# Optimization experiments

Measured on AMD Instinct MI355X. Metric: run time of the kernel, lower is better.

## Reference

```python
import jax, jax.numpy as jnp
import numpy as np
import math

B, S, D, H = 4, 2048, 1024, 16
HD = D // H  # head dim = 64


def setup_inputs() -> dict:
    key = jax.random.key(0)
    ks = jax.random.split(key, 8)
    queries = jax.random.normal(ks[0], (B, S, D), dtype=jnp.float32)
    keys = jax.random.normal(ks[1], (B, S, D), dtype=jnp.float32)
    values = jax.random.normal(ks[2], (B, S, D), dtype=jnp.float32)
    valid_lens = jnp.maximum(jax.random.randint(ks[3], (B,), 0, S), 1).astype(jnp.int64)
    scale = 1.0 / math.sqrt(D)
    Wq = jax.random.normal(ks[4], (H, D, HD), dtype=jnp.float32) * scale
    Wk = jax.random.normal(ks[5], (H, D, HD), dtype=jnp.float32) * scale
    Wv = jax.random.normal(ks[6], (H, D, HD), dtype=jnp.float32) * scale
    Wo = jax.random.normal(ks[7], (H * HD, D), dtype=jnp.float32) * scale
    return {"queries": queries, "keys": keys, "values": values,
            "valid_lens": valid_lens, "Wq": Wq, "Wk": Wk, "Wv": Wv, "Wo": Wo}


def reference(queries, keys, values, valid_lens, Wq, Wk, Wv, Wo):
    # Per-head projections, batched over heads: [B,S,D] x [H,D,HD] -> [B,H,S,HD]
    q = jnp.einsum('bsd,hde->bhse', queries, Wq)
    k = jnp.einsum('bsd,hde->bhse', keys, Wk)
    v = jnp.einsum('bsd,hde->bhse', values, Wv)
    # Scaled dot-product scores: [B,H,S,S]
    scores = jnp.einsum('bhse,bhte->bhst', q, k) / jnp.sqrt(jnp.float32(HD))
    # Padding mask only (causal=False default in the torch forward)
    pad = jnp.arange(S)[None, :] >= valid_lens[:, None]  # [B,S] True = masked
    scores = jnp.where(pad[:, None, None, :], -jnp.inf, scores)
    attn = jax.nn.softmax(scores, axis=-1)
    out = jnp.einsum('bhst,bhte->bhse', attn, v)  # [B,H,S,HD]
    out = out.transpose(0, 2, 1, 3).reshape(q.shape[0], S, H * HD)  # concat heads
    return out @ Wo
```

## Files before the change

### kernel.cpp

```cpp
#include <hip/hip_runtime.h>
#include <hip/hip_bf16.h>

typedef __bf16 bf16;
typedef __attribute__((ext_vector_type(8))) __bf16 bf16x8;
typedef __attribute__((ext_vector_type(4))) float f32x4;

#define DEV __device__ __forceinline__

DEV float fexp2(float x) {
#if __has_builtin(__builtin_amdgcn_exp2f)
  return __builtin_amdgcn_exp2f(x);
#else
  return exp2f(x);
#endif
}

DEV void gload_lds16(const void* g, void* l) {
  __builtin_amdgcn_global_load_lds(
      (__attribute__((address_space(1))) void*)(g),
      (__attribute__((address_space(3))) void*)(l), 16, 0, 0);
}

__global__ void k_cvt_act(const float* __restrict__ q, const float* __restrict__ k,
                          const float* __restrict__ v, bf16* __restrict__ qb,
                          bf16* __restrict__ kb, bf16* __restrict__ vb) {
  const int bid = blockIdx.x;
  const int which = bid >> 12;
  const float* in = which == 0 ? q : which == 1 ? k : v;
  bf16* out = which == 0 ? qb : which == 1 ? kb : vb;
  const int i = (bid & 4095) * 256 + threadIdx.x;
  const float4* p = reinterpret_cast<const float4*>(in) + (size_t)i * 2;
  float4 a = p[0], b = p[1];
  bf16x8 o;
  o[0] = (bf16)a.x; o[1] = (bf16)a.y; o[2] = (bf16)a.z; o[3] = (bf16)a.w;
  o[4] = (bf16)b.x; o[5] = (bf16)b.y; o[6] = (bf16)b.z; o[7] = (bf16)b.w;
  *reinterpret_cast<bf16x8*>(out + (size_t)i * 8) = o;
}

__global__ void k_cvt_w(const float* __restrict__ Wq, const float* __restrict__ Wk,
                        const float* __restrict__ Wv, const float* __restrict__ Wo,
                        bf16* __restrict__ WqkvT, bf16* __restrict__ WoT) {
  const int idx = blockIdx.x * blockDim.x + threadIdx.x;
  const int which = idx >> 20, r = idx & ((1 << 20) - 1);
  if (which < 3) {
    const float* W = which == 0 ? Wq : which == 1 ? Wk : Wv;
    const int d = r & 1023, n = r >> 10;
    float val = W[((size_t)(n >> 6) << 16) + (size_t)d * 64 + (n & 63)];
    if (which == 0) val *= 0.180336880f;
    WqkvT[((size_t)which << 20) + r] = (bf16)val;
  } else {
    const int kk = r & 1023, n = r >> 10;
    WoT[r] = (bf16)Wo[(size_t)kk * 1024 + n];
  }
}

__global__ __launch_bounds__(256) void k_gemm_qkv(const bf16* __restrict__ qA,
                                                  const bf16* __restrict__ kA,
                                                  const bf16* __restrict__ vA,
                                                  const bf16* __restrict__ Wt,
                                                  bf16* __restrict__ Qh,
                                                  bf16* __restrict__ Kh,
                                                  bf16* __restrict__ Vt) {
  constexpr int K = 1024;
  __shared__ __align__(16) bf16 As[128 * 32];
  __shared__ __align__(16) bf16 Bs[128 * 32];
  const int tid = threadIdx.x;
  const int lane = tid & 63, w = tid >> 6;
  const int wr = w >> 1, wc = w & 1;
  const int lgrp = lane >> 4, lid = lane & 15;
  const int m0 = blockIdx.x * 128;
  const int n0g = blockIdx.y * 128;
  const int proj = n0g >> 10, n0 = n0g & 1023;
  const bf16* A = proj == 0 ? qA : proj == 1 ? kA : vA;
  const bf16* Bt = Wt + (size_t)n0g * K;

  f32x4 acc[4][4] = {};

  const int c0 = w * 2, c1 = w * 2 + 1;
  const int bo0 = c0 * 1024 + lane * 16, bo1 = c1 * 1024 + lane * 16;
  const int r0 = bo0 >> 6, e0 = (bo0 & 63) >> 1;
  const int r1 = bo1 >> 6, e1 = (bo1 & 63) >> 1;

  for (int k0 = 0; k0 < K; k0 += 32) {
    __syncthreads();
    gload_lds16(A + (size_t)(m0 + r0) * K + k0 + e0, (char*)As + c0 * 1024);
    gload_lds16(A + (size_t)(m0 + r1) * K + k0 + e1, (char*)As + c1 * 1024);
    gload_lds16(Bt + (size_t)r0 * K + k0 + e0, (char*)Bs + c0 * 1024);
    gload_lds16(Bt + (size_t)r1 * K + k0 + e1, (char*)Bs + c1 * 1024);
    __syncthreads();
    bf16x8 af[4], bfv[4];
    for (int m = 0; m < 4; ++m)
      af[m] = *reinterpret_cast<const bf16x8*>(&As[(wr * 64 + m * 16 + lid) * 32 + lgrp * 8]);
    for (int n = 0; n < 4; ++n)
      bfv[n] = *reinterpret_cast<const bf16x8*>(&Bs[(wc * 64 + n * 16 + lid) * 32 + lgrp * 8]);
    for (int m = 0; m < 4; ++m)
      for (int n = 0; n < 4; ++n)
        acc[m][n] = __builtin_amdgcn_mfma_f32_16x16x32_bf16(af[m], bfv[n], acc[m][n], 0, 0, 0);
  }

  if (proj == 0) {
    for (int m = 0; m < 4; ++m) {
      int rowb = m0 + wr * 64 + m * 16 + lgrp * 4;
      for (int n = 0; n < 4; ++n) {
        int col = n0 + wc * 64 + n * 16 + lid;
        int h = col >> 6, e = col & 63;
        for (int r = 0; r < 4; ++r) {
          int row = rowb + r;
          int b = row >> 11, s = row & 2047;
          Qh[(((size_t)b * 16 + h) * 2048 + s) * 64 + e] = (bf16)acc[m][n][r];
        }
      }
    }
  } else if (proj == 1) {
    for (int m = 0; m < 4; ++m) {
      int rowb = m0 + wr * 64 + m * 16 + lgrp * 4;
      for (int n = 0; n < 4; ++n) {
        int col = n0 + wc * 64 + n * 16 + lid;
        int h = col >> 6, e = col & 63;
        for (int r = 0; r < 4; ++r) {
          int row = rowb + r;
          int b = row >> 11, s = row & 2047;
          Kh[(((size_t)b * 16 + h) * 2048 + s) * 64 + (e ^ ((s & 7) << 3))] = (bf16)acc[m][n][r];
        }
      }
    }
  } else {
    for (int m = 0; m < 4; ++m) {
      int rowb = m0 + wr * 64 + m * 16 + lgrp * 4;
      int b = rowb >> 11, s = rowb & 2047;
      for (int n = 0; n < 4; ++n) {
        int col = n0 + wc * 64 + n * 16 + lid;
        int h = col >> 6, e = col & 63;
        union { bf16 hv[4]; uint2 u; } tmp;
        for (int r = 0; r < 4; ++r) tmp.hv[r] = (bf16)acc[m][n][r];
        bf16* dst = Vt + (((size_t)b * 16 + h) * 64 + e) * 2048 + (s ^ ((e & 7) << 3));
        *reinterpret_cast<uint2*>(dst) = tmp.u;
      }
    }
  }
}

__global__ __launch_bounds__(256) void k_gemm_out(const bf16* __restrict__ A,
                                                  const bf16* __restrict__ Bt,
                                                  float* __restrict__ C) {
  constexpr int K = 1024;
  __shared__ __align__(16) bf16 As[128 * 32];
  __shared__ __align__(16) bf16 Bs[128 * 32];
  const int tid = threadIdx.x;
  const int lane = tid & 63, w = tid >> 6;
  const int wr = w >> 1, wc = w & 1;
  const int lgrp = lane >> 4, lid = lane & 15;
  const int m0 = blockIdx.x * 128, n0 = blockIdx.y * 128;

  f32x4 acc[4][4] = {};
  const int c0 = w * 2, c1 = w * 2 + 1;
  const int bo0 = c0 * 1024 + lane * 16, bo1 = c1 * 1024 + lane * 16;
  const int r0 = bo0 >> 6, e0 = (bo0 & 63) >> 1;
  const int r1 = bo1 >> 6, e1 = (bo1 & 63) >> 1;

  for (int k0 = 0; k0 < K; k0 += 32) {
    __syncthreads();
    gload_lds16(A + (size_t)(m0 + r0) * K + k0 + e0, (char*)As + c0 * 1024);
    gload_lds16(A + (size_t)(m0 + r1) * K + k0 + e1, (char*)As + c1 * 1024);
    gload_lds16(Bt + (size_t)(n0 + r0) * K + k0 + e0, (char*)Bs + c0 * 1024);
    gload_lds16(Bt + (size_t)(n0 + r1) * K + k0 + e1, (char*)Bs + c1 * 1024);
    __syncthreads();
    bf16x8 af[4], bfv[4];
    for (int m = 0; m < 4; ++m)
      af[m] = *reinterpret_cast<const bf16x8*>(&As[(wr * 64 + m * 16 + lid) * 32 + lgrp * 8]);
    for (int n = 0; n < 4; ++n)
      bfv[n] = *reinterpret_cast<const bf16x8*>(&Bs[(wc * 64 + n * 16 + lid) * 32 + lgrp * 8]);
    for (int m = 0; m < 4; ++m)
      for (int n = 0; n < 4; ++n)
        acc[m][n] = __builtin_amdgcn_mfma_f32_16x16x32_bf16(af[m], bfv[n], acc[m][n], 0, 0, 0);
  }
  for (int m = 0; m < 4; ++m) {
    int rowb = m0 + wr * 64 + m * 16 + lgrp * 4;
    for (int n = 0; n < 4; ++n) {
      int col = n0 + wc * 64 + n * 16 + lid;
      for (int r = 0; r < 4; ++r)
        C[(size_t)(rowb + r) * 1024 + col] = acc[m][n][r];
    }
  }
}

__global__ __launch_bounds__(512) void k_flash(const bf16* __restrict__ Qh,
                                               const bf16* __restrict__ Ksw,
                                               const bf16* __restrict__ Vsw,
                                               const int* __restrict__ valid,
                                               bf16* __restrict__ Ob) {
  __shared__ __align__(16) char Ks[2][64 * 128];
  __shared__ __align__(16) char Vs[2][64 * 128];
  __shared__ __align__(16) char Plds[8][16 * 128];
  const int tid = threadIdx.x, lane = tid & 63, w = tid >> 6;
  const int lgrp = lane >> 4, lid = lane & 15;
  const int blk = blockIdx.x;
  const int qt = blk & 15, bh = blk >> 4;
  const int b = bh >> 4, h = bh & 15;
  const int s0 = qt * 128 + w * 16;
  const bf16* Qp = Qh + ((size_t)bh * 2048 + s0) * 64;
  const bf16* Kp = Ksw + (size_t)bh * 2048 * 64;
  const bf16* Vp = Vsw + (size_t)bh * 64 * 2048;
  const int vl = valid[b];
  const int nt = (vl + 63) >> 6;
  const int full = vl >> 6;

  const int srow = 8 * w + (lane >> 3), col8 = (lane & 7) * 8;

  gload_lds16(Kp + (size_t)srow * 64 + col8, &Ks[0][(8 * w) * 128]);
  gload_lds16(Vp + (size_t)srow * 2048 + col8, &Vs[0][(8 * w) * 128]);

  bf16x8 aq0 = *reinterpret_cast<const bf16x8*>(Qp + lid * 64 + lgrp * 8);
  bf16x8 aq1 = *reinterpret_cast<const bf16x8*>(Qp + lid * 64 + 32 + lgrp * 8);

  f32x4 Of[4] = {};
  float mrow = -1e30f;
  float lpart = 0.f;
  char* Pw = &Plds[w][0];
  float* PwF = (float*)Pw;
  const int pswz = (lid & 7) << 4;

  int cur = 0;
  for (int t = 0; t < nt; ++t) {
    const int t0 = t * 64;
    __syncthreads();
    if (t + 1 < nt) {
      const int t1 = t0 + 64;
      gload_lds16(Kp + (size_t)(t1 + srow) * 64 + col8, &Ks[cur ^ 1][(8 * w) * 128]);
      gload_lds16(Vp + (size_t)srow * 2048 + t1 + col8, &Vs[cur ^ 1][(8 * w) * 128]);
    }
    f32x4 sc[4] = {};
#pragma unroll
    for (int ct = 0; ct < 4; ++ct) {
      const int row = ct * 16 + lid;
      const char* kb = &Ks[cur][row * 128];
      const int msk = (row & 7) << 4;
      bf16x8 bk0 = *reinterpret_cast<const bf16x8*>(kb + ((lgrp * 16) ^ msk));
      bf16x8 bk1 = *reinterpret_cast<const bf16x8*>(kb + ((64 + lgrp * 16) ^ msk));
      sc[ct] = __builtin_amdgcn_mfma_f32_16x16x32_bf16(bk0, aq0, sc[ct], 0, 0, 0);
      sc[ct] = __builtin_amdgcn_mfma_f32_16x16x32_bf16(bk1, aq1, sc[ct], 0, 0, 0);
    }
    if (t >= full) {
#pragma unroll
      for (int ct = 0; ct < 4; ++ct)
#pragma unroll
        for (int r = 0; r < 4; ++r)
          sc[ct][r] = (t0 + ct * 16 + lgrp * 4 + r) >= vl ? -1e30f : sc[ct][r];
    }
    float vm = fmaxf(fmaxf(fmaxf(sc[0][0], sc[0][1]), fmaxf(sc[0][2], sc[0][3])),
                     fmaxf(fmaxf(sc[1][0], sc[1][1]), fmaxf(sc[1][2], sc[1][3])));
    vm = fmaxf(vm, fmaxf(fmaxf(fmaxf(sc[2][0], sc[2][1]), fmaxf(sc[2][2], sc[2][3])),
                         fmaxf(fmaxf(sc[3][0], sc[3][1]), fmaxf(sc[3][2], sc[3][3]))));
    if (__any(vm > mrow + 8.f)) {
      vm = fmaxf(vm, __shfl_xor(vm, 16));
      vm = fmaxf(vm, __shfl_xor(vm, 32));
      float mnew = fmaxf(mrow, vm);
      float scl = fexp2(mrow - mnew);
      mrow = mnew;
      lpart *= scl;
      if (lgrp == 0) PwF[lid] = scl;
      asm volatile("s_waitcnt lgkmcnt(0)" ::: "memory");
      f32x4 sq = *reinterpret_cast<const f32x4*>(PwF + lgrp * 4);
#pragma unroll
      for (int f = 0; f < 4; ++f)
#pragma unroll
        for (int r = 0; r < 4; ++r)
          Of[f][r] *= sq[r];
    }
#pragma unroll
    for (int ct = 0; ct < 4; ++ct)
#pragma unroll
      for (int r = 0; r < 4; ++r)
        sc[ct][r] = fexp2(sc[ct][r] - mrow);
#pragma unroll
    for (int ct = 0; ct < 4; ++ct) {
      union { bf16 hv[2]; unsigned int u; } p0, p1;
      p0.hv[0] = (bf16)sc[ct][0]; p0.hv[1] = (bf16)sc[ct][1];
      p1.hv[0] = (bf16)sc[ct][2]; p1.hv[1] = (bf16)sc[ct][3];
      char* base = Pw + lid * 128 + (((ct * 32 + lgrp * 8)) ^ pswz);
      *reinterpret_cast<unsigned int*>(base) = p0.u;
      *reinterpret_cast<unsigned int*>(base + 4) = p1.u;
    }
    asm volatile("s_waitcnt lgkmcnt(0)" ::: "memory");
    bf16x8 pa0 = *reinterpret_cast<const bf16x8*>(Pw + lid * 128 + ((lgrp * 16) ^ pswz));
    bf16x8 pa1 = *reinterpret_cast<const bf16x8*>(Pw + lid * 128 + ((64 + lgrp * 16) ^ pswz));
#pragma unroll
    for (int f = 0; f < 4; ++f) {
      const int row = f * 16 + lid;
      const char* vb = &Vs[cur][row * 128];
      const int msk = (row & 7) << 4;
      bf16x8 bv0 = *reinterpret_cast<const bf16x8*>(vb + ((lgrp * 16) ^ msk));
      bf16x8 bv1 = *reinterpret_cast<const bf16x8*>(vb + ((64 + lgrp * 16) ^ msk));
      Of[f] = __builtin_amdgcn_mfma_f32_16x16x32_bf16(pa0, bv0, Of[f], 0, 0, 0);
      Of[f] = __builtin_amdgcn_mfma_f32_16x16x32_bf16(pa1, bv1, Of[f], 0, 0, 0);
    }
    lpart += ((sc[0][0] + sc[0][1]) + (sc[0][2] + sc[0][3])) +
             ((sc[1][0] + sc[1][1]) + (sc[1][2] + sc[1][3])) +
             ((sc[2][0] + sc[2][1]) + (sc[2][2] + sc[2][3])) +
             ((sc[3][0] + sc[3][1]) + (sc[3][2] + sc[3][3]));
    cur ^= 1;
  }
  float l = lpart;
  l += __shfl_xor(l, 16);
  l += __shfl_xor(l, 32);
  float inv = 1.f / l;
  if (lgrp == 0) PwF[lid] = inv;
  asm volatile("s_waitcnt lgkmcnt(0)" ::: "memory");
  f32x4 invq = *reinterpret_cast<const f32x4*>(PwF + lgrp * 4);
  bf16* Op = Ob + ((size_t)b * 2048 + s0) * 1024 + h * 64;
#pragma unroll
  for (int r = 0; r < 4; ++r)
#pragma unroll
    for (int f = 0; f < 4; ++f)
      Op[(size_t)(lgrp * 4 + r) * 1024 + f * 16 + lid] = (bf16)(Of[f][r] * invq[r]);
}

extern "C" void kernel_launch(void* const* d_in, const int* in_sizes, int n_in,
                              void* d_out, int out_size, void* d_ws, size_t ws_size,
                              hipStream_t stream) {
  const float* q = (const float*)d_in[0];
  const float* k = (const float*)d_in[1];
  const float* v = (const float*)d_in[2];
  const int* vl = (const int*)d_in[3];
  const float* Wq = (const float*)d_in[4];
  const float* Wk = (const float*)d_in[5];
  const float* Wv = (const float*)d_in[6];
  const float* Wo = (const float*)d_in[7];

  char* ws = (char*)d_ws;
  const size_t SZW = (size_t)1024 * 1024 * 2;
  const size_t SZT = (size_t)8192 * 1024 * 2;
  bf16* WqkvT = (bf16*)(ws);
  bf16* WoT = (bf16*)(ws + 3 * SZW);
  bf16* Qh  = (bf16*)(ws + 4 * SZW);
  bf16* Kh  = (bf16*)(ws + 4 * SZW + SZT);
  bf16* Vt  = (bf16*)(ws + 4 * SZW + 2 * SZT);
  bf16* qb  = (bf16*)(ws + 4 * SZW + 3 * SZT);
  bf16* kb  = (bf16*)(ws + 4 * SZW + 4 * SZT);
  bf16* vb  = (bf16*)(ws + 4 * SZW + 5 * SZT);
  bf16* attnb = qb;

  k_cvt_act<<<12288, 256, 0, stream>>>(q, k, v, qb, kb, vb);
  k_cvt_w<<<16384, 256, 0, stream>>>(Wq, Wk, Wv, Wo, WqkvT, WoT);
  dim3 gq(64, 24);
  k_gemm_qkv<<<gq, 256, 0, stream>>>(qb, kb, vb, WqkvT, Qh, Kh, Vt);
  k_flash<<<1024, 512, 0, stream>>>(Qh, Kh, Vt, vl, attnb);
  dim3 go(64, 8);
  k_gemm_out<<<go, 256, 0, stream>>>(attnb, WoT, (float*)d_out);
}
```

Baseline: 205.8 us.

## Rewrite QKV projection GEMM with 256x256 tiles, double-buffered swizzled LDS pipeline

The QKV projection GEMM moves from 128x128 tiles with K-step 32 and two barriers per step to 256x256 tiles with K-step 64 and 512 threads. LDS is double-buffered with an XOR swizzle, and loads for the next tiles are issued in phases interleaved with the MFMA work, with vmcnt waits and raised wave priority around the MFMAs. A remapped block index groups work by XCD. The aim is to hide global-load latency, avoid LDS bank conflicts and raise operand reuse, at the cost of more LDS and registers per block and only 384 blocks.

```diff
diff --git a/kernel.cpp b/kernel.cpp
--- a/kernel.cpp
+++ b/kernel.cpp
@@ -20,6 +20,11 @@
       (__attribute__((address_space(1))) void*)(g),
       (__attribute__((address_space(3))) void*)(l), 16, 0, 0);
 }
+
+template <int N>
+DEV void waitvm() { asm volatile("s_waitcnt vmcnt(%0)" ::"n"(N) : "memory"); }
+DEV void fence() { asm volatile("" ::: "memory"); }
+DEV void bar() { fence(); __builtin_amdgcn_s_barrier(); fence(); }
 
 __global__ void k_cvt_act(const float* __restrict__ q, const float* __restrict__ k,
                           const float* __restrict__ v, bf16* __restrict__ qb,
@@ -54,86 +59,142 @@
   }
 }
 
-__global__ __launch_bounds__(256) void k_gemm_qkv(const bf16* __restrict__ qA,
-                                                  const bf16* __restrict__ kA,
-                                                  const bf16* __restrict__ vA,
-                                                  const bf16* __restrict__ Wt,
-                                                  bf16* __restrict__ Qh,
-                                                  bf16* __restrict__ Kh,
-                                                  bf16* __restrict__ Vt) {
-  constexpr int K = 1024;
-  __shared__ __align__(16) bf16 As[128 * 32];
-  __shared__ __align__(16) bf16 Bs[128 * 32];
-  const int tid = threadIdx.x;
-  const int lane = tid & 63, w = tid >> 6;
-  const int wr = w >> 1, wc = w & 1;
+DEV void stage_half(const bf16* __restrict__ srcb, bf16 (*lds)[64], int h, int k0,
+                    int tid) {
+  const int wv = tid >> 6;
+#pragma unroll
+  for (int l = 0; l < 2; ++l) {
+    const int row = h * 128 + l * 64 + (tid >> 3);
+    const int e = (((tid & 7) ^ (row & 7)) << 3);
+    gload_lds16(srcb + (size_t)row * 1024 + k0 + e,
+                (char*)&lds[h * 128 + l * 64][0] + wv * 1024);
+  }
+}
+
+DEV bf16x8 ldsfrag(const bf16 (*lds)[64], int row, int kk, int lgrp) {
+  const int ch = ((kk << 2) + lgrp) ^ (row & 7);
+  return *reinterpret_cast<const bf16x8*>((const char*)&lds[row][0] + (ch << 4));
+}
+
+__global__ __launch_bounds__(512, 2) void k_gemm_qkv(const bf16* __restrict__ qA,
+                                                     const bf16* __restrict__ kA,
+                                                     const bf16* __restrict__ vA,
+                                                     const bf16* __restrict__ Wt,
+                                                     bf16* __restrict__ Qh,
+                                                     bf16* __restrict__ Kh,
+                                                     bf16* __restrict__ Vt) {
+  __shared__ __align__(16) bf16 AsB[2][256][64];
+  __shared__ __align__(16) bf16 BsB[2][256][64];
+  const int tid = threadIdx.x, lane = tid & 63, w = tid >> 6;
   const int lgrp = lane >> 4, lid = lane & 15;
-  const int m0 = blockIdx.x * 128;
-  const int n0g = blockIdx.y * 128;
-  const int proj = n0g >> 10, n0 = n0g & 1023;
+  const int wr = w >> 2, wn = w & 3;
+  const int bid0 = blockIdx.x;
+  const int bid = (bid0 & 7) * 48 + (bid0 >> 3);
+  const int proj = bid >> 7;
+  const int rem = bid & 127;
+  const int mt = rem >> 2, ntl = rem & 3;
+  const int m0 = mt * 256, n0 = ntl * 256;
   const bf16* A = proj == 0 ? qA : proj == 1 ? kA : vA;
-  const bf16* Bt = Wt + (size_t)n0g * K;
-
-  f32x4 acc[4][4] = {};
-
-  const int c0 = w * 2, c1 = w * 2 + 1;
-  const int bo0 = c0 * 1024 + lane * 16, bo1 = c1 * 1024 + lane * 16;
-  const int r0 = bo0 >> 6, e0 = (bo0 & 63) >> 1;
-  const int r1 = bo1 >> 6, e1 = (bo1 & 63) >> 1;
-
-  for (int k0 = 0; k0 < K; k0 += 32) {
-    __syncthreads();
-    gload_lds16(A + (size_t)(m0 + r0) * K + k0 + e0, (char*)As + c0 * 1024);
-    gload_lds16(A + (size_t)(m0 + r1) * K + k0 + e1, (char*)As + c1 * 1024);
-    gload_lds16(Bt + (size_t)r0 * K + k0 + e0, (char*)Bs + c0 * 1024);
-    gload_lds16(Bt + (size_t)r1 * K + k0 + e1, (char*)Bs + c1 * 1024);
-    __syncthreads();
-    bf16x8 af[4], bfv[4];
-    for (int m = 0; m < 4; ++m)
-      af[m] = *reinterpret_cast<const bf16x8*>(&As[(wr * 64 + m * 16 + lid) * 32 + lgrp * 8]);
-    for (int n = 0; n < 4; ++n)
-      bfv[n] = *reinterpret_cast<const bf16x8*>(&Bs[(wc * 64 + n * 16 + lid) * 32 + lgrp * 8]);
-    for (int m = 0; m < 4; ++m)
-      for (int n = 0; n < 4; ++n)
-        acc[m][n] = __builtin_amdgcn_mfma_f32_16x16x32_bf16(af[m], bfv[n], acc[m][n], 0, 0, 0);
-  }
-
+  const bf16* Am = A + (size_t)m0 * 1024;
+  const bf16* Bt = Wt + ((size_t)proj * 1024 + n0) * 1024;
+
+  f32x4 acc[8][4] = {};
+  constexpr int NT = 16;
+
+  stage_half(Am, AsB[0], 0, 0, tid);
+  stage_half(Am, AsB[0], 1, 0, tid);
+  stage_half(Bt, BsB[0], 0, 0, tid);
+  stage_half(Bt, BsB[0], 1, 0, tid);
+  stage_half(Bt, BsB[1], 0, 64, tid);
+  stage_half(Bt, BsB[1], 1, 64, tid);
+  waitvm<4>();
+  bar();
+
+  int cur = 0;
+  for (int kt = 0; kt < NT; ++kt) {
+    bf16x8 bfr[4][2];
+#pragma unroll
+    for (int p = 0; p < 4; ++p) {
+      if (p == 0) {
+#pragma unroll
+        for (int n = 0; n < 4; ++n)
+#pragma unroll
+          for (int kk = 0; kk < 2; ++kk)
+            bfr[n][kk] = ldsfrag(BsB[cur], wn * 64 + n * 16 + lid, kk, lgrp);
+      }
+      bf16x8 afr[2][2];
+#pragma unroll
+      for (int mi = 0; mi < 2; ++mi)
+#pragma unroll
+        for (int kk = 0; kk < 2; ++kk)
+          afr[mi][kk] = ldsfrag(AsB[cur], wr * 128 + (p * 2 + mi) * 16 + lid, kk, lgrp);
+      if (p < 2) {
+        if (kt + 1 < NT) stage_half(Am, AsB[cur ^ 1], p, (kt + 1) * 64, tid);
+      } else {
+        if (kt + 2 < NT) stage_half(Bt, BsB[cur], p - 2, (kt + 2) * 64, tid);
+      }
+      bar();
+      __builtin_amdgcn_s_setprio(1);
+#pragma unroll
+      for (int mi = 0; mi < 2; ++mi)
+#pragma unroll
+        for (int n = 0; n < 4; ++n)
+#pragma unroll
+          for (int kk = 0; kk < 2; ++kk)
+            acc[p * 2 + mi][n] = __builtin_amdgcn_mfma_f32_16x16x32_bf16(
+                afr[mi][kk], bfr[n][kk], acc[p * 2 + mi][n], 0, 0, 0);
+      __builtin_amdgcn_s_setprio(0);
+      if (p == 3) {
+        if (kt < NT - 2) waitvm<4>();
+        else if (kt == NT - 2) waitvm<0>();
+      }
+      bar();
+    }
+    cur ^= 1;
+  }
+
+  const int hh = (n0 >> 6) + wn;
   if (proj == 0) {
-    for (int m = 0; m < 4; ++m) {
-      int rowb = m0 + wr * 64 + m * 16 + lgrp * 4;
+#pragma unroll
+    for (int mm = 0; mm < 8; ++mm) {
+      const int rowb = m0 + wr * 128 + mm * 16 + lgrp * 4;
+      const int bb = rowb >> 11, s = rowb & 2047;
+#pragma unroll
       for (int n = 0; n < 4; ++n) {
-        int col = n0 + wc * 64 + n * 16 + lid;
-        int h = col >> 6, e = col & 63;
+        const int e = n * 16 + lid;
+        bf16* dst = Qh + (((size_t)bb * 16 + hh) * 2048 + s) * 64 + e;
+#pragma unroll
+        for (int r = 0; r < 4; ++r) dst[(size_t)r * 64] = (bf16)acc[mm][n][r];
+      }
+    }
+  } else if (proj == 1) {
+#pragma unroll
+    for (int mm = 0; mm < 8; ++mm) {
+      const int rowb = m0 + wr * 128 + mm * 16 + lgrp * 4;
+      const int bb = rowb >> 11, s = rowb & 2047;
+#pragma unroll
+      for (int n = 0; n < 4; ++n) {
+        const int e = n * 16 + lid;
+#pragma unroll
         for (int r = 0; r < 4; ++r) {
-          int row = rowb + r;
-          int b = row >> 11, s = row & 2047;
-          Qh[(((size_t)b * 16 + h) * 2048 + s) * 64 + e] = (bf16)acc[m][n][r];
+          const int sr = s + r;
+          Kh[(((size_t)bb * 16 + hh) * 2048 + sr) * 64 + (e ^ ((sr & 7) << 3))] =
+              (bf16)acc[mm][n][r];
         }
       }
     }
-  } else if (proj == 1) {
-    for (int m = 0; m < 4; ++m) {
-      int rowb = m0 + wr * 64 + m * 16 + lgrp * 4;
+  } else {
+#pragma unroll
+    for (int mm = 0; mm < 8; ++mm) {
+      const int rowb = m0 + wr * 128 + mm * 16 + lgrp * 4;
+      const int bb = rowb >> 11, s = rowb & 2047;
+#pragma unroll
       for (int n = 0; n < 4; ++n) {
-        int col = n0 + wc * 64 + n * 16 + lid;
-        int h = col >> 6, e = col & 63;
-        for (int r = 0; r < 4; ++r) {
-          int row = rowb + r;
-          int b = row >> 11, s = row & 2047;
-          Kh[(((size_t)b * 16 + h) * 2048 + s) * 64 + (e ^ ((s & 7) << 3))] = (bf16)acc[m][n][r];
-        }
-      }
-    }
-  } else {
-    for (int m = 0; m < 4; ++m) {
-      int rowb = m0 + wr * 64 + m * 16 + lgrp * 4;
-      int b = rowb >> 11, s = rowb & 2047;
-      for (int n = 0; n < 4; ++n) {
-        int col = n0 + wc * 64 + n * 16 + lid;
-        int h = col >> 6, e = col & 63;
+        const int e = n * 16 + lid;
         union { bf16 hv[4]; uint2 u; } tmp;
-        for (int r = 0; r < 4; ++r) tmp.hv[r] = (bf16)acc[m][n][r];
-        bf16* dst = Vt + (((size_t)b * 16 + h) * 64 + e) * 2048 + (s ^ ((e & 7) << 3));
+#pragma unroll
+        for (int r = 0; r < 4; ++r) tmp.hv[r] = (bf16)acc[mm][n][r];
+        bf16* dst = Vt + (((size_t)bb * 16 + hh) * 64 + e) * 2048 + (s ^ ((e & 7) << 3));
         *reinterpret_cast<uint2*>(dst) = tmp.u;
       }
     }
@@ -342,8 +403,7 @@
 
   k_cvt_act<<<12288, 256, 0, stream>>>(q, k, v, qb, kb, vb);
   k_cvt_w<<<16384, 256, 0, stream>>>(Wq, Wk, Wv, Wo, WqkvT, WoT);
-  dim3 gq(64, 24);
-  k_gemm_qkv<<<gq, 256, 0, stream>>>(qb, kb, vb, WqkvT, Qh, Kh, Vt);
+  k_gemm_qkv<<<384, 512, 0, stream>>>(qb, kb, vb, WqkvT, Qh, Kh, Vt);
   k_flash<<<1024, 512, 0, stream>>>(Qh, Kh, Vt, vl, attnb);
   dim3 go(64, 8);
   k_gemm_out<<<go, 256, 0, stream>>>(attnb, WoT, (float*)d_out);
```

New measurement: 212.2 us. 3.1% more time.
